# Kernel optimization log

Measured on AMD Instinct MI355X. Metric: run time of the kernel, lower is better.

Reference implementation:

```python
import jax, jax.numpy as jnp
import numpy as np

RANGE0 = -3.0   # x/y offset of grid
VOX = 6.0       # voxel size -> nx = ny = 1
EPS_BN = 1e-3   # BatchNorm eps used in PFN / conv head
EPS_MLP = 1e-5  # default BN eps inside pyg-style MLP


def _bn_masked(h, w, gamma, beta, eps):
    # training-mode BatchNorm1d over valid rows only (w is [N,1] 0/1 mask)
    n = jnp.maximum(w.sum(), 1.0)
    m = (h * w).sum(0) / n
    v = (jnp.square(h - m) * w).sum(0) / n
    return (h - m) * jax.lax.rsqrt(v + eps) * gamma + beta


def _bn(h, gamma, beta, eps):
    # training-mode BatchNorm over axis 0 (spatial dims are 1x1)
    m = h.mean(0)
    v = jnp.square(h - m).mean(0)
    return (h - m) * jax.lax.rsqrt(v + eps) * gamma + beta


def _pillar_branch(x, batch, B, W1, g1, bb1, W2, g2, bb2):
    # dynamic voxelization: grid is 1x1, so pillar id == batch id for in-range points
    pts, extra = x[:, :3], x[:, 3:]
    cx = jnp.floor((pts[:, 0] - RANGE0) / VOX)
    cy = jnp.floor((pts[:, 1] - RANGE0) / VOX)
    valid = (cx >= 0) & (cx < 1) & (cy >= 0) & (cy < 1)
    seg = jnp.where(valid, batch, B).astype(jnp.int32)  # invalid -> dummy segment B
    w = valid.astype(x.dtype)[:, None]

    cnt = jax.ops.segment_sum(w[:, 0], seg, num_segments=B + 1)        # [B+1]
    psum = jax.ops.segment_sum(pts * w, seg, num_segments=B + 1)       # [B+1,3]
    pmean = psum / jnp.maximum(cnt, 1.0)[:, None]
    f_cluster = pts - pmean[seg]                                        # [N,3]
    f_center = jnp.stack([pts[:, 0] - (cx * VOX + RANGE0),
                          pts[:, 1] - (cy * VOX + RANGE0),
                          pts[:, 2]], axis=1)                           # [N,3]
    feat = jnp.concatenate([pts, f_cluster, f_center, extra], axis=1)  # [N,12]

    # PFN layer 1: Lin(12,32,no bias) + BN + ReLU + scatter_max + concat -> [N,64]
    h = feat @ W1
    h = jax.nn.relu(_bn_masked(h, w, g1, bb1, EPS_BN))
    hmax = jax.ops.segment_max(h, seg, num_segments=B + 1)
    hmax = jnp.where(jnp.isfinite(hmax), hmax, 0.0)
    h = jnp.concatenate([h, hmax[seg]], axis=1)                        # [N,64]

    # PFN layer 2 (last): Lin(64,64,no bias) + BN + ReLU + scatter_max -> [B,64]
    h = h @ W2
    h = jax.nn.relu(_bn_masked(h, w, g2, bb2, EPS_BN))
    pmax = jax.ops.segment_max(h, seg, num_segments=B + 1)[:B]
    pmax = jnp.where((cnt[:B] > 0)[:, None],
                     jnp.where(jnp.isfinite(pmax), pmax, 0.0), 0.0)
    return pmax  # BEV features, grid is 1x1 so scatter_to_bev == identity


def setup_inputs() -> dict:
    key = jax.random.key(0)
    ks = jax.random.split(key, 10)
    N, B = 500000, 64
    x = jax.random.normal(ks[0], (N, 6), jnp.float32)
    x2 = jax.random.normal(ks[1], (N, 6), jnp.float32)
    batch = jnp.sort(jax.random.randint(ks[2], (N,), 0, B)).astype(jnp.int32)
    batch2 = jnp.sort(jax.random.randint(ks[3], (N,), 0, B)).astype(jnp.int32)
    y = jax.random.randint(ks[4], (B,), 0, 5).astype(jnp.int32)

    def w(k, shape, fan_in):
        return (jax.random.normal(k, shape, jnp.float32) / np.sqrt(fan_in)).astype(jnp.float32)

    return dict(
        x=x, x2=x2, batch=batch, batch2=batch2, y=y,
        W1=w(ks[5], (12, 32), 12), g1=jnp.ones(32, jnp.float32), bb1=jnp.zeros(32, jnp.float32),
        W2=w(ks[6], (64, 64), 64), g2=jnp.ones(64, jnp.float32), bb2=jnp.zeros(64, jnp.float32),
        Wc=w(ks[7], (1024, 64), 64), gc=jnp.ones(1024, jnp.float32), bc=jnp.zeros(1024, jnp.float32),
        Wm1=w(ks[8], (1024, 64), 1024), bm1=jnp.zeros(64, jnp.float32),
        gm=jnp.ones(64, jnp.float32), bm=jnp.zeros(64, jnp.float32),
        Wm2=w(ks[9], (64, 5), 64), bm2=jnp.zeros(5, jnp.float32),
    )


def reference(x, x2, batch, batch2, y,
              W1, g1, bb1, W2, g2, bb2,
              Wc, gc, bc, Wm1, bm1, gm, bm, Wm2, bm2):
    B = y.shape[0]
    p1 = _pillar_branch(x, batch, B, W1, g1, bb1, W2, g2, bb2)    # [B,64]
    p2 = _pillar_branch(x2, batch2, B, W1, g1, bb1, W2, g2, bb2)  # [B,64]
    # conv_2d: 1x1 conv 64->1024 on 1x1 BEV == linear, + BN2d + ReLU
    z1 = jax.nn.relu(_bn(p1 @ Wc.T, gc, bc, EPS_BN))              # [B,1024]
    z2 = jax.nn.relu(_bn(p2 @ Wc.T, gc, bc, EPS_BN))
    d = z2 - z1
    # MLP([1024,64]) = Lin + ReLU + BN, then Lin(64,5)
    h = _bn(jax.nn.relu(d @ Wm1 + bm1), gm, bm, EPS_MLP)
    logits = h @ Wm2 + bm2
    return jax.nn.log_softmax(logits, axis=-1)
```

## Files before the change

### kernel.cpp

```cpp
#include <hip/hip_runtime.h>
#include <float.h>
#include <math.h>

#define S0 4
#define SB 8

#define O_BOUNDS 0
#define O_W2BF   160
#define BR_BASE  1184
#define O_CNT    0
#define O_BIASP  64
#define O_UP     2112
#define O_P0PART 2304
#define O_SEGSR  9472
#define O_SEGZMX 11520
#define O_SEGSQ  13568
#define O_SEGMMX 17664
#define O_PMAX   21760
#define BRSZ     25856
#define O_D      (BR_BASE + 2*BRSZ)
#define O_HMLP   (O_D + 65536)

typedef __attribute__((ext_vector_type(8))) short short8;
typedef __attribute__((ext_vector_type(4))) float f32x4;

__device__ __forceinline__ void atomicMaxF(float* a, float v) {
    if (v >= 0.f) atomicMax((int*)a, __float_as_int(v));
    else atomicMin((unsigned int*)a, (unsigned int)__float_as_int(v));
}
__device__ __forceinline__ bool is_valid(float p0, float p1) {
    return (floorf((p0 + 3.f) / 6.f) == 0.f) && (floorf((p1 + 3.f) / 6.f) == 0.f);
}
__device__ __forceinline__ unsigned short f2bf(float x) {
    unsigned int u = __float_as_uint(x);
    return (unsigned short)((u + 0x7FFFu + ((u >> 16) & 1u)) >> 16);
}

__global__ __launch_bounds__(256) void segBoundsKernel(const int* __restrict__ bt0, const int* __restrict__ bt1,
                                                       int N, float* ws) {
    int br = blockIdx.y;
    const int* batch = br ? bt1 : bt0;
    float* base = ws + BR_BASE + (size_t)br * BRSZ;
    int* bounds = (int*)(ws + O_BOUNDS) + br * 65;
    int gid = blockIdx.x * 256 + threadIdx.x;
    int stride = gridDim.x * 256;
    for (int i = gid; i < N; i += stride) {
        int b = batch[i];
        int prev = (i == 0) ? -1 : batch[i - 1];
        for (int v = prev + 1; v <= b; v++) bounds[v] = i;
        if (i == N - 1) for (int v = b + 1; v <= 64; v++) bounds[v] = N;
    }
    if (blockIdx.x == 0) {
        int t = threadIdx.x;
        #pragma unroll
        for (int r = 0; r < 8; r++) {
            int idx = t + r * 256;
            base[O_SEGSR + idx] = 0.f;
            base[O_SEGZMX + idx] = 0.f;
        }
        #pragma unroll
        for (int r = 0; r < 16; r++) {
            int idx = t + r * 256;
            base[O_SEGSQ + idx] = 0.f;
            base[O_SEGMMX + idx] = 0.f;
        }
    }
}

__global__ __launch_bounds__(256) void pass0Kernel(const float* __restrict__ x0,
                                                   const float* __restrict__ x1,
                                                   int N, float* ws) {
    int br = blockIdx.y;
    const float* x = br ? x1 : x0;
    float* base = ws + BR_BASE + (size_t)br * BRSZ;
    const int* bounds = (const int*)(ws + O_BOUNDS) + br * 65;
    int b = blockIdx.x / S0, s = blockIdx.x % S0;
    int lo = bounds[b], hi = bounds[b + 1];
    int chunk = (hi - lo + S0 - 1) / S0;
    int beg = lo + s * chunk, end = min(hi, beg + chunk);

    float acc[28];
    #pragma unroll
    for (int k = 0; k < 28; k++) acc[k] = 0.f;

    int i0 = beg + (int)threadIdx.x;
    float2 a0, a1, a2;
    {
        int ip = max(min(i0, end - 1), 0);
        const float2* pp = (const float2*)(x + (size_t)ip * 6);
        a0 = pp[0]; a1 = pp[1]; a2 = pp[2];
    }
    for (int i = i0; i < end; i += 256) {
        float2 c0 = a0, c1 = a1, c2 = a2;
        int ipn = max(min(i + 256, end - 1), 0);
        const float2* pp = (const float2*)(x + (size_t)ipn * 6);
        a0 = pp[0]; a1 = pp[1]; a2 = pp[2];
        float f[6] = {c0.x, c0.y, c1.x, c1.y, c2.x, c2.y};
        if (is_valid(f[0], f[1])) {
            acc[0] += 1.f;
            #pragma unroll
            for (int k = 0; k < 6; k++) acc[1 + k] += f[k];
            int k = 7;
            #pragma unroll
            for (int a = 0; a < 6; a++)
                #pragma unroll
                for (int c = a; c < 6; c++) { acc[k] = fmaf(f[a], f[c], acc[k]); k++; }
        }
    }
    __shared__ float red[4][28];
    int w = threadIdx.x >> 6, l = threadIdx.x & 63;
    #pragma unroll
    for (int k = 0; k < 28; k++) {
        float v = acc[k];
        v += __shfl_xor(v, 1); v += __shfl_xor(v, 2); v += __shfl_xor(v, 4);
        v += __shfl_xor(v, 8); v += __shfl_xor(v, 16); v += __shfl_xor(v, 32);
        acc[k] = v;
    }
    if (l == 0) { for (int k = 0; k < 28; k++) red[w][k] = acc[k]; }
    __syncthreads();
    if (threadIdx.x < 28) {
        float v = red[0][threadIdx.x] + red[1][threadIdx.x] + red[2][threadIdx.x] + red[3][threadIdx.x];
        base[O_P0PART + (size_t)(b * S0 + s) * 28 + threadIdx.x] = v;
    }
}

__global__ __launch_bounds__(256) void bn1CoefKernel(const float* __restrict__ W1,
                                                     const float* __restrict__ W2,
                                                     const float* __restrict__ g1,
                                                     const float* __restrict__ bb1, float* ws) {
    int br = blockIdx.y;
    float* base = ws + BR_BASE + (size_t)br * BRSZ;
    int t = threadIdx.x;
    __shared__ float SEG[64][28];
    __shared__ float Ul[6][32];
    __shared__ float BIASS[64][32];
    __shared__ float aS[32], abS[32];
    __shared__ float red[8][32], red2[8][32];

    if (t < 192) {
        int k = t / 32, c = t & 31;
        Ul[k][c] = (k < 3) ? (W1[k*32+c] + W1[(k+3)*32+c] + W1[(k+6)*32+c]) : W1[(k+6)*32+c];
    }
    #pragma unroll
    for (int r = 0; r < 4; r++) {
        int idx = t + r * 256;
        unsigned int lo = f2bf(W2[2*idx]), hi = f2bf(W2[2*idx + 1]);
        ((unsigned int*)(ws + O_W2BF))[idx] = lo | (hi << 16);
    }
    #pragma unroll
    for (int r = 0; r < 7; r++) {
        int idx = t + r * 256;
        int b = idx / 28, k = idx % 28;
        float v = 0.f;
        for (int sc = 0; sc < S0; sc++) v += base[O_P0PART + (size_t)(b*S0+sc)*28 + k];
        SEG[b][k] = v;
    }
    __syncthreads();
    if (t < 64) base[O_CNT + t] = SEG[t][0];

    int c = t & 31, bg = t >> 5;
    float c32 = 3.f * (W1[6*32+c] + W1[7*32+c]);
    float ps1 = 0.f, pss = 0.f;
    for (int j = 0; j < 8; j++) {
        int b = bg * 8 + j;
        float cnt = SEG[b][0];
        float cn = fmaxf(cnt, 1.f);
        float bias = c32 - (SEG[b][1]/cn)*W1[3*32+c] - (SEG[b][2]/cn)*W1[4*32+c] - (SEG[b][3]/cn)*W1[5*32+c];
        BIASS[b][c] = bias;
        float dotv = 0.f;
        #pragma unroll
        for (int i = 0; i < 6; i++) dotv = fmaf(SEG[b][1+i], Ul[i][c], dotv);
        float quad = 0.f;
        int k = 7;
        #pragma unroll
        for (int i = 0; i < 6; i++) {
            quad = fmaf(SEG[b][k], Ul[i][c] * Ul[i][c], quad); k++;
            #pragma unroll
            for (int j2 = i + 1; j2 < 6; j2++) { quad = fmaf(SEG[b][k], 2.f * Ul[i][c] * Ul[j2][c], quad); k++; }
        }
        ps1 += dotv + cnt * bias;
        pss += quad + 2.f * bias * dotv + cnt * bias * bias;
    }
    red[bg][c] = ps1; red2[bg][c] = pss;
    __syncthreads();
    if (bg == 0) {
        float s1 = 0.f, sq = 0.f;
        for (int k = 0; k < 8; k++) { s1 += red[k][c]; sq += red2[k][c]; }
        float tot = 0.f;
        for (int k = 0; k < 64; k++) tot += SEG[k][0];
        float n = fmaxf(tot, 1.f);
        float m = s1 / n, v = sq / n - m * m;
        float a = g1[c] * rsqrtf(v + 0.001f);
        aS[c] = a; abS[c] = bb1[c] - m * a;
    }
    __syncthreads();
    if (t < 192) {
        int cc = t & 31;
        base[O_UP + t] = aS[cc] * Ul[t / 32][cc];
    }
    #pragma unroll
    for (int r = 0; r < 8; r++) {
        int idx = t + r * 256;
        int cc = idx & 31;
        base[O_BIASP + idx] = fmaf(aS[cc], BIASS[idx >> 5][cc], abS[cc]);
    }
}

__global__ __launch_bounds__(256) void passBKernel(const float* __restrict__ x0,
                                                   const float* __restrict__ x1,
                                                   int N, float* ws) {
    int br = blockIdx.y;
    const float* x = br ? x1 : x0;
    float* base = ws + BR_BASE + (size_t)br * BRSZ;
    const int* bounds = (const int*)(ws + O_BOUNDS) + br * 65;
    int b = blockIdx.x / SB, s = blockIdx.x % SB;
    int lo = bounds[b], hi = bounds[b + 1];
    int chunk = (hi - lo + SB - 1) / SB;
    int beg = lo + s * chunk, end = min(hi, beg + chunk);
    int npts = end - beg;
    int ntiles = npts > 0 ? ((npts + 63) >> 6) : 0;
    int ntiles3 = ((ntiles + 2) / 3) * 3;

    int t = threadIdx.x;
    int w = t >> 6, l = t & 63, n0 = l & 15, g4 = l >> 4;
    int myoff = 16 * w + n0;
    int c8 = 8 * g4;

    const unsigned short* w2u = (const unsigned short*)(ws + O_W2BF);
    short8 bfrag[4];
    #pragma unroll
    for (int ct = 0; ct < 4; ct++)
        #pragma unroll
        for (int j = 0; j < 8; j++)
            bfrag[ct][j] = (short)w2u[(c8 + j) * 64 + 16 * ct + n0];

    float uj[8][6], biasp[8];
    #pragma unroll
    for (int j = 0; j < 8; j++) {
        #pragma unroll
        for (int k = 0; k < 6; k++) uj[j][k] = base[O_UP + k * 32 + c8 + j];
        biasp[j] = base[O_BIASP + b * 32 + c8 + j];
    }

    float srelu[8], rmx[8];
    #pragma unroll
    for (int j = 0; j < 8; j++) { srelu[j] = 0.f; rmx[j] = 0.f; }
    f32x4 sq[4], mxa[4];
    #pragma unroll
    for (int ct = 0; ct < 4; ct++) {
        sq[ct] = (f32x4){0, 0, 0, 0};
        mxa[ct] = (f32x4){0, 0, 0, 0};
    }

    float2 xa0, xa1, xa2, xb0, xb1, xb2, xc0, xc1, xc2;
#define LOADP(d0, d1, d2, tk) do { \
        int idxc_ = beg + (tk) * 64 + myoff; \
        int idxl_ = max(min(idxc_, end - 1), 0); \
        const float2* px_ = (const float2*)(x + (size_t)idxl_ * 6); \
        d0 = px_[0]; d1 = px_[1]; d2 = px_[2]; } while (0)

#define PROCESS(q0, q1, q2, tk) do { \
        float p0 = q0.x, p1 = q0.y, p2 = q1.x, e0 = q1.y, e1 = q2.x, e2 = q2.y; \
        bool val = (beg + (tk) * 64 + myoff < end) && is_valid(p0, p1); \
        float r8[8]; \
        _Pragma("unroll") \
        for (int j = 0; j < 8; j++) { \
            float z = fmaf(p0, uj[j][0], fmaf(p1, uj[j][1], fmaf(p2, uj[j][2], \
                      fmaf(e0, uj[j][3], fmaf(e1, uj[j][4], fmaf(e2, uj[j][5], biasp[j])))))); \
            float r = fmaxf(z, 0.f); \
            r = val ? r : 0.f; \
            srelu[j] += r; \
            rmx[j] = fmaxf(rmx[j], r); \
            r8[j] = r; \
        } \
        unsigned int pk0, pk1, pk2, pk3; \
        asm("v_cvt_pk_bf16_f32 %0, %1, %2" : "=v"(pk0) : "v"(r8[0]), "v"(r8[1])); \
        asm("v_cvt_pk_bf16_f32 %0, %1, %2" : "=v"(pk1) : "v"(r8[2]), "v"(r8[3])); \
        asm("v_cvt_pk_bf16_f32 %0, %1, %2" : "=v"(pk2) : "v"(r8[4]), "v"(r8[5])); \
        asm("v_cvt_pk_bf16_f32 %0, %1, %2" : "=v"(pk3) : "v"(r8[6]), "v"(r8[7])); \
        uint4 pkv; pkv.x = pk0; pkv.y = pk1; pkv.z = pk2; pkv.w = pk3; \
        short8 af = __builtin_bit_cast(short8, pkv); \
        _Pragma("unroll") \
        for (int ct = 0; ct < 4; ct++) { \
            f32x4 cz = (f32x4){0, 0, 0, 0}; \
            f32x4 v = __builtin_amdgcn_mfma_f32_16x16x32_bf16(af, bfrag[ct], cz, 0, 0, 0); \
            _Pragma("unroll") \
            for (int r = 0; r < 4; r++) { \
                sq[ct][r] = fmaf(v[r], v[r], sq[ct][r]); \
                mxa[ct][r] = fmaxf(mxa[ct][r], v[r]); \
            } \
        } } while (0)

    if (ntiles3 > 0) {
        LOADP(xa0, xa1, xa2, 0);
        LOADP(xb0, xb1, xb2, 1);
        LOADP(xc0, xc1, xc2, 2);
        for (int k = 0; k < ntiles3; k += 3) {
            float2 ta0 = xa0, ta1 = xa1, ta2 = xa2;
            LOADP(xa0, xa1, xa2, k + 3);
            PROCESS(ta0, ta1, ta2, k);
            float2 tb0 = xb0, tb1 = xb1, tb2 = xb2;
            LOADP(xb0, xb1, xb2, k + 4);
            PROCESS(tb0, tb1, tb2, k + 1);
            float2 tc0 = xc0, tc1 = xc1, tc2 = xc2;
            LOADP(xc0, xc1, xc2, k + 5);
            PROCESS(tc0, tc1, tc2, k + 2);
        }
    }
#undef LOADP
#undef PROCESS

    __shared__ float redA[4][32], redB[4][32], redC[4][64], redD[4][64];
    float sred[8], zred[8];
    #pragma unroll
    for (int j = 0; j < 8; j++) {
        float sv = srelu[j], zv = rmx[j];
        sv += __shfl_xor(sv, 1); sv += __shfl_xor(sv, 2); sv += __shfl_xor(sv, 4); sv += __shfl_xor(sv, 8);
        zv = fmaxf(zv, __shfl_xor(zv, 1)); zv = fmaxf(zv, __shfl_xor(zv, 2));
        zv = fmaxf(zv, __shfl_xor(zv, 4)); zv = fmaxf(zv, __shfl_xor(zv, 8));
        sred[j] = sv; zred[j] = zv;
    }
    if (n0 == 0) {
        #pragma unroll
        for (int j = 0; j < 8; j++) { redA[w][c8 + j] = sred[j]; redB[w][c8 + j] = zred[j]; }
    }
    float sqs[4], mxs[4];
    #pragma unroll
    for (int ct = 0; ct < 4; ct++) {
        float sv = sq[ct][0] + sq[ct][1] + sq[ct][2] + sq[ct][3];
        float mv = fmaxf(fmaxf(mxa[ct][0], mxa[ct][1]), fmaxf(mxa[ct][2], mxa[ct][3]));
        sv += __shfl_xor(sv, 16); sv += __shfl_xor(sv, 32);
        mv = fmaxf(mv, __shfl_xor(mv, 16)); mv = fmaxf(mv, __shfl_xor(mv, 32));
        sqs[ct] = sv; mxs[ct] = mv;
    }
    if (l < 16) {
        #pragma unroll
        for (int ct = 0; ct < 4; ct++) { redC[w][16 * ct + l] = sqs[ct]; redD[w][16 * ct + l] = mxs[ct]; }
    }
    __syncthreads();
    if (t < 32) {
        atomicAdd(&base[O_SEGSR + b * 32 + t], redA[0][t] + redA[1][t] + redA[2][t] + redA[3][t]);
    } else if (t < 64) {
        int c = t - 32;
        float v = fmaxf(fmaxf(redB[0][c], redB[1][c]), fmaxf(redB[2][c], redB[3][c]));
        atomicMaxF(&base[O_SEGZMX + b * 32 + c], v);
    } else if (t < 128) {
        int c = t - 64;
        atomicAdd(&base[O_SEGSQ + b * 64 + c], redC[0][c] + redC[1][c] + redC[2][c] + redC[3][c]);
    } else if (t < 192) {
        int c = t - 128;
        float v = fmaxf(fmaxf(redD[0][c], redD[1][c]), fmaxf(redD[2][c], redD[3][c]));
        atomicMaxF(&base[O_SEGMMX + b * 64 + c], v);
    }
}

__global__ __launch_bounds__(256) void segFuseKernel(const float* __restrict__ W2,
                                                     const float* __restrict__ g2,
                                                     const float* __restrict__ bb2, float* ws) {
    int br = blockIdx.y;
    float* base = ws + BR_BASE + (size_t)br * BRSZ;
    int t = threadIdx.x;
    __shared__ float HM[64][32], SR[64][32];
    __shared__ float W2a[32][64], W2b[32][64];
    __shared__ float HS[64][64];
    __shared__ float CNTl[64];
    __shared__ float redS[4][64], redQ[4][64];
    __shared__ float AB2[2][64];

    #pragma unroll
    for (int r = 0; r < 8; r++) {
        int idx = t + r * 256;
        ((float*)W2a)[idx] = W2[idx];
        ((float*)W2b)[idx] = W2[2048 + idx];
    }
    if (t < 64) CNTl[t] = base[O_CNT + t];
    #pragma unroll
    for (int r = 0; r < 8; r++) {
        int idx = t + r * 256;
        int b = idx >> 5, c = idx & 31;
        SR[b][c] = base[O_SEGSR + idx];
        HM[b][c] = base[O_SEGZMX + idx];
    }
    __syncthreads();
    int col = t & 63, bgq = t >> 6;
    float S = 0.f, Q = 0.f;
    for (int j = 0; j < 16; j++) {
        int b = bgq * 16 + j;
        float hs = 0.f, smm = 0.f;
        #pragma unroll
        for (int ch = 0; ch < 32; ch++) {
            hs  = fmaf(HM[b][ch], W2b[ch][col], hs);
            smm = fmaf(SR[b][ch], W2a[ch][col], smm);
        }
        HS[b][col] = hs;
        float cnt = CNTl[b];
        float qb = base[O_SEGSQ + b * 64 + col];
        S += smm + cnt * hs;
        Q += qb + 2.f * hs * smm + cnt * hs * hs;
    }
    redS[bgq][col] = S; redQ[bgq][col] = Q;
    __syncthreads();
    if (t < 64) {
        float Sv = redS[0][t] + redS[1][t] + redS[2][t] + redS[3][t];
        float Qv = redQ[0][t] + redQ[1][t] + redQ[2][t] + redQ[3][t];
        float tot = 0.f;
        for (int k = 0; k < 64; k++) tot += CNTl[k];
        float n = fmaxf(tot, 1.f);
        float m = Sv / n, v = Qv / n - m * m;
        float a = g2[t] * rsqrtf(v + 0.001f);
        AB2[0][t] = a; AB2[1][t] = bb2[t] - m * a;
    }
    __syncthreads();
    #pragma unroll
    for (int r = 0; r < 16; r++) {
        int idx = t + r * 256;
        int b = idx >> 6, c2 = idx & 63;
        float mv = base[O_SEGMMX + b * 64 + c2];
        float out = 0.f;
        if (CNTl[b] > 0.f) out = fmaxf(fmaf(AB2[0][c2], mv + HS[b][c2], AB2[1][c2]), 0.f);
        base[O_PMAX + b * 64 + c2] = out;
    }
}

__global__ __launch_bounds__(256) void dKernel(const float* __restrict__ Wc, const float* __restrict__ gc,
                                               const float* __restrict__ bc, float* ws) {
    __shared__ float P1s[64 * 65], P2s[64 * 65], WcS[4][64];
    int t = threadIdx.x;
    const float* p1 = ws + BR_BASE + O_PMAX;
    const float* p2 = ws + BR_BASE + BRSZ + O_PMAX;
    #pragma unroll
    for (int r = 0; r < 16; r++) {
        int idx = t + r * 256;
        int i2 = idx >> 6, c2 = idx & 63;
        P1s[i2 * 65 + c2] = p1[idx];
        P2s[i2 * 65 + c2] = p2[idx];
    }
    int jl = t >> 6, i = t & 63;
    int j = blockIdx.x * 4 + jl;
    WcS[jl][i] = Wc[(size_t)j * 64 + i];
    __syncthreads();
    float t1 = 0.f, t2 = 0.f;
    #pragma unroll
    for (int c = 0; c < 64; c++) {
        float wv = WcS[jl][c];
        t1 = fmaf(P1s[i * 65 + c], wv, t1);
        t2 = fmaf(P2s[i * 65 + c], wv, t2);
    }
    float m1 = t1, m2 = t2;
    for (int off = 32; off; off >>= 1) { m1 += __shfl_xor(m1, off); m2 += __shfl_xor(m2, off); }
    m1 *= (1.f / 64.f); m2 *= (1.f / 64.f);
    float d1 = t1 - m1, d2 = t2 - m2;
    float v1 = d1 * d1, v2 = d2 * d2;
    for (int off = 32; off; off >>= 1) { v1 += __shfl_xor(v1, off); v2 += __shfl_xor(v2, off); }
    v1 *= (1.f / 64.f); v2 *= (1.f / 64.f);
    float z1 = fmaxf(d1 * rsqrtf(v1 + 0.001f) * gc[j] + bc[j], 0.f);
    float z2 = fmaxf(d2 * rsqrtf(v2 + 0.001f) * gc[j] + bc[j], 0.f);
    ws[O_D + (size_t)j * 64 + i] = z2 - z1;
}

__global__ __launch_bounds__(256) void hKernel(const float* __restrict__ Wm1, const float* __restrict__ bm1,
                                               const float* __restrict__ gm, const float* __restrict__ bm,
                                               float* ws) {
    int cidx = blockIdx.x;
    int t = threadIdx.x;
    int i = t & 63, q = t >> 6;
    const float* dT = ws + O_D;
    float part = 0.f;
    for (int k = q * 256; k < q * 256 + 256; k++)
        part = fmaf(dT[(size_t)k * 64 + i], Wm1[(size_t)k * 64 + cidx], part);
    __shared__ float red[4][64];
    red[q][i] = part; __syncthreads();
    if (t < 64) {
        float u = red[0][t] + red[1][t] + red[2][t] + red[3][t] + bm1[cidx];
        u = fmaxf(u, 0.f);
        float m = u;
        for (int off = 32; off; off >>= 1) m += __shfl_xor(m, off);
        m *= (1.f / 64.f);
        float du = u - m;
        float v = du * du;
        for (int off = 32; off; off >>= 1) v += __shfl_xor(v, off);
        v *= (1.f / 64.f);
        ws[O_HMLP + (size_t)t * 64 + cidx] = du * rsqrtf(v + 1e-5f) * gm[cidx] + bm[cidx];
    }
}

__global__ void outKernel(const float* __restrict__ Wm2, const float* __restrict__ bm2,
                          const float* __restrict__ ws, float* out) {
    __shared__ float lg[64][5];
    __shared__ float lse[64];
    int t = threadIdx.x;
    {
        int i = t / 5, j = t % 5;
        const float* h = ws + O_HMLP;
        float acc = bm2[j];
        for (int k = 0; k < 64; k++) acc = fmaf(h[i * 64 + k], Wm2[k * 5 + j], acc);
        lg[i][j] = acc;
    }
    __syncthreads();
    if (t < 64) {
        float mxv = lg[t][0];
        for (int j = 1; j < 5; j++) mxv = fmaxf(mxv, lg[t][j]);
        float sv = 0.f;
        for (int j = 0; j < 5; j++) sv += expf(lg[t][j] - mxv);
        lse[t] = mxv + logf(sv);
    }
    __syncthreads();
    out[t] = lg[t / 5][t % 5] - lse[t / 5];
}

extern "C" void kernel_launch(void* const* d_in, const int* in_sizes, int n_in,
                              void* d_out, int out_size, void* d_ws, size_t ws_size,
                              hipStream_t stream) {
    const float* x0  = (const float*)d_in[0];
    const float* x1  = (const float*)d_in[1];
    const int*   bt0 = (const int*)d_in[2];
    const int*   bt1 = (const int*)d_in[3];
    const float* W1  = (const float*)d_in[5];
    const float* g1  = (const float*)d_in[6];
    const float* bb1 = (const float*)d_in[7];
    const float* W2  = (const float*)d_in[8];
    const float* g2  = (const float*)d_in[9];
    const float* bb2 = (const float*)d_in[10];
    const float* Wc  = (const float*)d_in[11];
    const float* gc  = (const float*)d_in[12];
    const float* bc  = (const float*)d_in[13];
    const float* Wm1 = (const float*)d_in[14];
    const float* bm1 = (const float*)d_in[15];
    const float* gm  = (const float*)d_in[16];
    const float* bm  = (const float*)d_in[17];
    const float* Wm2 = (const float*)d_in[18];
    const float* bm2 = (const float*)d_in[19];
    float* ws  = (float*)d_ws;
    float* out = (float*)d_out;
    int N = in_sizes[0] / 6;

    segBoundsKernel<<<dim3(128, 2),    dim3(256), 0, stream>>>(bt0, bt1, N, ws);
    pass0Kernel    <<<dim3(64*S0, 2),  dim3(256), 0, stream>>>(x0, x1, N, ws);
    bn1CoefKernel  <<<dim3(1, 2),      dim3(256), 0, stream>>>(W1, W2, g1, bb1, ws);
    passBKernel    <<<dim3(64*SB, 2),  dim3(256), 0, stream>>>(x0, x1, N, ws);
    segFuseKernel  <<<dim3(1, 2),      dim3(256), 0, stream>>>(W2, g2, bb2, ws);
    dKernel        <<<dim3(256),       dim3(256), 0, stream>>>(Wc, gc, bc, ws);
    hKernel        <<<dim3(64),        dim3(256), 0, stream>>>(Wm1, bm1, gm, bm, ws);
    outKernel      <<<dim3(1),         dim3(320), 0, stream>>>(Wm2, bm2, ws, out);
}
```

Before: 86.42 us.

## Fuse single-block BN coefficient kernels into producers via last-block-done counters

Removes the two single-block kernels (bn1Coef and segFuse) by running their work in whichever block of pass0/passB finishes last, found through an atomic done-counter per branch. The W2 bf16 conversion moves into segBoundsKernel, and passB gets a launch-bounds occupancy hint. This cuts two kernel launches and their gaps, at the cost of extra fences and atomics, a larger shared-memory footprint in the producer kernels, and a serialized tail run by one block.

```diff
diff --git a/kernel.cpp b/kernel.cpp
--- a/kernel.cpp
+++ b/kernel.cpp
@@ -7,7 +7,8 @@
 
 #define O_BOUNDS 0
 #define O_W2BF   160
-#define BR_BASE  1184
+#define O_DONE   1184
+#define BR_BASE  1188
 #define O_CNT    0
 #define O_BIASP  64
 #define O_UP     2112
@@ -24,6 +25,9 @@
 typedef __attribute__((ext_vector_type(8))) short short8;
 typedef __attribute__((ext_vector_type(4))) float f32x4;
 
+#define ALOAD(p)     __hip_atomic_load((p), __ATOMIC_RELAXED, __HIP_MEMORY_SCOPE_AGENT)
+#define ASTORE(p, v) __hip_atomic_store((p), (v), __ATOMIC_RELAXED, __HIP_MEMORY_SCOPE_AGENT)
+
 __device__ __forceinline__ void atomicMaxF(float* a, float v) {
     if (v >= 0.f) atomicMax((int*)a, __float_as_int(v));
     else atomicMin((unsigned int*)a, (unsigned int)__float_as_int(v));
@@ -37,7 +41,7 @@
 }
 
 __global__ __launch_bounds__(256) void segBoundsKernel(const int* __restrict__ bt0, const int* __restrict__ bt1,
-                                                       int N, float* ws) {
+                                                       const float* __restrict__ W2, int N, float* ws) {
     int br = blockIdx.y;
     const int* batch = br ? bt1 : bt0;
     float* base = ws + BR_BASE + (size_t)br * BRSZ;
@@ -64,12 +68,29 @@
             base[O_SEGSQ + idx] = 0.f;
             base[O_SEGMMX + idx] = 0.f;
         }
+        if (threadIdx.x == 0) {
+            ((unsigned*)(ws + O_DONE))[br] = 0u;
+            ((unsigned*)(ws + O_DONE))[2 + br] = 0u;
+        }
+    }
+    if (blockIdx.x == 1 && br == 0) {
+        int t = threadIdx.x;
+        #pragma unroll
+        for (int r = 0; r < 4; r++) {
+            int idx = t + r * 256;
+            unsigned int lo = f2bf(W2[2 * idx]), hi = f2bf(W2[2 * idx + 1]);
+            ((unsigned int*)(ws + O_W2BF))[idx] = lo | (hi << 16);
+        }
     }
 }
 
 __global__ __launch_bounds__(256) void pass0Kernel(const float* __restrict__ x0,
                                                    const float* __restrict__ x1,
-                                                   int N, float* ws) {
+                                                   int N,
+                                                   const float* __restrict__ W1,
+                                                   const float* __restrict__ g1,
+                                                   const float* __restrict__ bb1,
+                                                   float* ws) {
     int br = blockIdx.y;
     const float* x = br ? x1 : x0;
     float* base = ws + BR_BASE + (size_t)br * BRSZ;
@@ -120,40 +141,38 @@
     __syncthreads();
     if (threadIdx.x < 28) {
         float v = red[0][threadIdx.x] + red[1][threadIdx.x] + red[2][threadIdx.x] + red[3][threadIdx.x];
-        base[O_P0PART + (size_t)(b * S0 + s) * 28 + threadIdx.x] = v;
-    }
-}
-
-__global__ __launch_bounds__(256) void bn1CoefKernel(const float* __restrict__ W1,
-                                                     const float* __restrict__ W2,
-                                                     const float* __restrict__ g1,
-                                                     const float* __restrict__ bb1, float* ws) {
-    int br = blockIdx.y;
-    float* base = ws + BR_BASE + (size_t)br * BRSZ;
+        ASTORE(&base[O_P0PART + (size_t)(b * S0 + s) * 28 + threadIdx.x], v);
+    }
+    __syncthreads();
+    __threadfence();
+    __shared__ int lastFlag;
+    if (threadIdx.x == 0) {
+        unsigned old = atomicAdd(((unsigned*)(ws + O_DONE)) + br, 1u);
+        lastFlag = (old == (unsigned)(64 * S0 - 1)) ? 1 : 0;
+    }
+    __syncthreads();
+    if (!lastFlag) return;
+    __threadfence();
+
     int t = threadIdx.x;
     __shared__ float SEG[64][28];
     __shared__ float Ul[6][32];
     __shared__ float BIASS[64][32];
     __shared__ float aS[32], abS[32];
-    __shared__ float red[8][32], red2[8][32];
+    __shared__ float redp[8][32], redq[8][32];
 
     if (t < 192) {
         int k = t / 32, c = t & 31;
         Ul[k][c] = (k < 3) ? (W1[k*32+c] + W1[(k+3)*32+c] + W1[(k+6)*32+c]) : W1[(k+6)*32+c];
     }
     #pragma unroll
-    for (int r = 0; r < 4; r++) {
-        int idx = t + r * 256;
-        unsigned int lo = f2bf(W2[2*idx]), hi = f2bf(W2[2*idx + 1]);
-        ((unsigned int*)(ws + O_W2BF))[idx] = lo | (hi << 16);
-    }
-    #pragma unroll
     for (int r = 0; r < 7; r++) {
         int idx = t + r * 256;
-        int b = idx / 28, k = idx % 28;
+        int b2 = idx / 28, k = idx % 28;
         float v = 0.f;
-        for (int sc = 0; sc < S0; sc++) v += base[O_P0PART + (size_t)(b*S0+sc)*28 + k];
-        SEG[b][k] = v;
+        for (int sc = 0; sc < S0; sc++)
+            v += ALOAD(&base[O_P0PART + (size_t)(b2 * S0 + sc) * 28 + k]);
+        SEG[b2][k] = v;
     }
     __syncthreads();
     if (t < 64) base[O_CNT + t] = SEG[t][0];
@@ -162,30 +181,30 @@
     float c32 = 3.f * (W1[6*32+c] + W1[7*32+c]);
     float ps1 = 0.f, pss = 0.f;
     for (int j = 0; j < 8; j++) {
-        int b = bg * 8 + j;
-        float cnt = SEG[b][0];
+        int b2 = bg * 8 + j;
+        float cnt = SEG[b2][0];
         float cn = fmaxf(cnt, 1.f);
-        float bias = c32 - (SEG[b][1]/cn)*W1[3*32+c] - (SEG[b][2]/cn)*W1[4*32+c] - (SEG[b][3]/cn)*W1[5*32+c];
-        BIASS[b][c] = bias;
+        float bias = c32 - (SEG[b2][1]/cn)*W1[3*32+c] - (SEG[b2][2]/cn)*W1[4*32+c] - (SEG[b2][3]/cn)*W1[5*32+c];
+        BIASS[b2][c] = bias;
         float dotv = 0.f;
         #pragma unroll
-        for (int i = 0; i < 6; i++) dotv = fmaf(SEG[b][1+i], Ul[i][c], dotv);
+        for (int i = 0; i < 6; i++) dotv = fmaf(SEG[b2][1+i], Ul[i][c], dotv);
         float quad = 0.f;
         int k = 7;
         #pragma unroll
         for (int i = 0; i < 6; i++) {
-            quad = fmaf(SEG[b][k], Ul[i][c] * Ul[i][c], quad); k++;
+            quad = fmaf(SEG[b2][k], Ul[i][c] * Ul[i][c], quad); k++;
             #pragma unroll
-            for (int j2 = i + 1; j2 < 6; j2++) { quad = fmaf(SEG[b][k], 2.f * Ul[i][c] * Ul[j2][c], quad); k++; }
+            for (int j2 = i + 1; j2 < 6; j2++) { quad = fmaf(SEG[b2][k], 2.f * Ul[i][c] * Ul[j2][c], quad); k++; }
         }
         ps1 += dotv + cnt * bias;
         pss += quad + 2.f * bias * dotv + cnt * bias * bias;
     }
-    red[bg][c] = ps1; red2[bg][c] = pss;
+    redp[bg][c] = ps1; redq[bg][c] = pss;
     __syncthreads();
     if (bg == 0) {
         float s1 = 0.f, sq = 0.f;
-        for (int k = 0; k < 8; k++) { s1 += red[k][c]; sq += red2[k][c]; }
+        for (int k = 0; k < 8; k++) { s1 += redp[k][c]; sq += redq[k][c]; }
         float tot = 0.f;
         for (int k = 0; k < 64; k++) tot += SEG[k][0];
         float n = fmaxf(tot, 1.f);
@@ -206,9 +225,13 @@
     }
 }
 
-__global__ __launch_bounds__(256) void passBKernel(const float* __restrict__ x0,
-                                                   const float* __restrict__ x1,
-                                                   int N, float* ws) {
+__global__ __launch_bounds__(256, 4) void passBKernel(const float* __restrict__ x0,
+                                                      const float* __restrict__ x1,
+                                                      int N,
+                                                      const float* __restrict__ W2,
+                                                      const float* __restrict__ g2,
+                                                      const float* __restrict__ bb2,
+                                                      float* ws) {
     int br = blockIdx.y;
     const float* x = br ? x1 : x0;
     float* base = ws + BR_BASE + (size_t)br * BRSZ;
@@ -352,14 +375,18 @@
         float v = fmaxf(fmaxf(redD[0][c], redD[1][c]), fmaxf(redD[2][c], redD[3][c]));
         atomicMaxF(&base[O_SEGMMX + b * 64 + c], v);
     }
-}
-
-__global__ __launch_bounds__(256) void segFuseKernel(const float* __restrict__ W2,
-                                                     const float* __restrict__ g2,
-                                                     const float* __restrict__ bb2, float* ws) {
-    int br = blockIdx.y;
-    float* base = ws + BR_BASE + (size_t)br * BRSZ;
-    int t = threadIdx.x;
+
+    __syncthreads();
+    __threadfence();
+    __shared__ int lastFlag;
+    if (t == 0) {
+        unsigned old = atomicAdd(((unsigned*)(ws + O_DONE)) + 2 + br, 1u);
+        lastFlag = (old == (unsigned)(64 * SB - 1)) ? 1 : 0;
+    }
+    __syncthreads();
+    if (!lastFlag) return;
+    __threadfence();
+
     __shared__ float HM[64][32], SR[64][32];
     __shared__ float W2a[32][64], W2b[32][64];
     __shared__ float HS[64][64];
@@ -377,24 +404,24 @@
     #pragma unroll
     for (int r = 0; r < 8; r++) {
         int idx = t + r * 256;
-        int b = idx >> 5, c = idx & 31;
-        SR[b][c] = base[O_SEGSR + idx];
-        HM[b][c] = base[O_SEGZMX + idx];
+        int b2 = idx >> 5, c = idx & 31;
+        SR[b2][c] = ALOAD(&base[O_SEGSR + idx]);
+        HM[b2][c] = ALOAD(&base[O_SEGZMX + idx]);
     }
     __syncthreads();
     int col = t & 63, bgq = t >> 6;
     float S = 0.f, Q = 0.f;
     for (int j = 0; j < 16; j++) {
-        int b = bgq * 16 + j;
+        int b2 = bgq * 16 + j;
         float hs = 0.f, smm = 0.f;
         #pragma unroll
         for (int ch = 0; ch < 32; ch++) {
-            hs  = fmaf(HM[b][ch], W2b[ch][col], hs);
-            smm = fmaf(SR[b][ch], W2a[ch][col], smm);
-        }
-        HS[b][col] = hs;
-        float cnt = CNTl[b];
-        float qb = base[O_SEGSQ + b * 64 + col];
+            hs  = fmaf(HM[b2][ch], W2b[ch][col], hs);
+            smm = fmaf(SR[b2][ch], W2a[ch][col], smm);
+        }
+        HS[b2][col] = hs;
+        float cnt = CNTl[b2];
+        float qb = ALOAD(&base[O_SEGSQ + b2 * 64 + col]);
         S += smm + cnt * hs;
         Q += qb + 2.f * hs * smm + cnt * hs * hs;
     }
@@ -414,11 +441,11 @@
     #pragma unroll
     for (int r = 0; r < 16; r++) {
         int idx = t + r * 256;
-        int b = idx >> 6, c2 = idx & 63;
-        float mv = base[O_SEGMMX + b * 64 + c2];
-        float out = 0.f;
-        if (CNTl[b] > 0.f) out = fmaxf(fmaf(AB2[0][c2], mv + HS[b][c2], AB2[1][c2]), 0.f);
-        base[O_PMAX + b * 64 + c2] = out;
+        int b2 = idx >> 6, c2 = idx & 63;
+        float mv = ALOAD(&base[O_SEGMMX + b2 * 64 + c2]);
+        float outv = 0.f;
+        if (CNTl[b2] > 0.f) outv = fmaxf(fmaf(AB2[0][c2], mv + HS[b2][c2], AB2[1][c2]), 0.f);
+        base[O_PMAX + b2 * 64 + c2] = outv;
     }
 }
 
@@ -534,11 +561,9 @@
     float* out = (float*)d_out;
     int N = in_sizes[0] / 6;
 
-    segBoundsKernel<<<dim3(128, 2),    dim3(256), 0, stream>>>(bt0, bt1, N, ws);
-    pass0Kernel    <<<dim3(64*S0, 2),  dim3(256), 0, stream>>>(x0, x1, N, ws);
-    bn1CoefKernel  <<<dim3(1, 2),      dim3(256), 0, stream>>>(W1, W2, g1, bb1, ws);
-    passBKernel    <<<dim3(64*SB, 2),  dim3(256), 0, stream>>>(x0, x1, N, ws);
-    segFuseKernel  <<<dim3(1, 2),      dim3(256), 0, stream>>>(W2, g2, bb2, ws);
+    segBoundsKernel<<<dim3(128, 2),    dim3(256), 0, stream>>>(bt0, bt1, W2, N, ws);
+    pass0Kernel    <<<dim3(64*S0, 2),  dim3(256), 0, stream>>>(x0, x1, N, W1, g1, bb1, ws);
+    passBKernel    <<<dim3(64*SB, 2),  dim3(256), 0, stream>>>(x0, x1, N, W2, g2, bb2, ws);
     dKernel        <<<dim3(256),       dim3(256), 0, stream>>>(Wc, gc, bc, ws);
     hKernel        <<<dim3(64),        dim3(256), 0, stream>>>(Wm1, bm1, gm, bm, ws);
     outKernel      <<<dim3(1),         dim3(320), 0, stream>>>(Wm2, bm2, ws, out);
```

Result: slower. 184.3 us (+113.2%).
